# Optimization experiments

Hardware: AMD Instinct MI355X
Metric: run time of the kernel (lower is better)

Reference implementation:

```python
import jax, jax.numpy as jnp
import numpy as np

N = 50000
E = 800000
IN_CH = 128
HID = 32
HEADS = 8
OUT_CH = 64
NEG_SLOPE = 0.2


def _gat_layer(x, W, att_src, att_dst, bias, src, dst, H, C, concat):
    """One GATConv layer (add aggregation, self-loops appended).
    x: [n, Fin], W: [Fin, H*C], att_*: [H, C], bias: [H*C] or [C].
    src/dst: [E] int edge endpoints (no self loops; they are appended here).
    """
    n = x.shape[0]
    xs = (x @ W).reshape(n, H, C)                 # projected features [n,H,C]
    a_src = (xs * att_src).sum(-1)                # [n,H]
    a_dst = (xs * att_dst).sum(-1)                # [n,H]
    loop = jnp.arange(n, dtype=src.dtype)
    s = jnp.concatenate([src, loop])              # [E+n]
    d = jnp.concatenate([dst, loop])
    alpha = a_src[s] + a_dst[d]                   # per-edge score [E+n,H]
    alpha = jax.nn.leaky_relu(alpha, NEG_SLOPE)
    # segment softmax over destination node (every node has a self loop,
    # so no empty segments)
    amax = jax.ops.segment_max(alpha, d, num_segments=n)
    ex = jnp.exp(alpha - amax[d])
    denom = jax.ops.segment_sum(ex, d, num_segments=n)
    alpha = ex / denom[d]                         # normalized attention [E+n,H]
    # weighted scatter-add aggregation
    out = jax.ops.segment_sum(alpha[:, :, None] * xs[s], d, num_segments=n)
    out = out.reshape(n, H * C) if concat else out.mean(axis=1)
    return out + bias


def setup_inputs() -> dict:
    key = jax.random.key(0)
    ks = jax.random.split(key, 12)
    def glorot(k, shape):
        fan = shape[0] + shape[-1]
        return jax.random.uniform(k, shape, jnp.float32,
                                  -jnp.sqrt(6.0 / fan), jnp.sqrt(6.0 / fan))
    x = jax.random.normal(ks[0], (N, IN_CH), jnp.float32)
    edge_index = jax.random.randint(ks[1], (2, E), 0, N, dtype=jnp.int64)
    W1 = glorot(ks[2], (IN_CH, HEADS * HID))
    att_src1 = glorot(ks[3], (HEADS, HID))
    att_dst1 = glorot(ks[4], (HEADS, HID))
    bias1 = jnp.zeros((HEADS * HID,), jnp.float32)
    W2 = glorot(ks[5], (HEADS * HID, 1 * OUT_CH))
    att_src2 = glorot(ks[6], (1, OUT_CH))
    att_dst2 = glorot(ks[7], (1, OUT_CH))
    bias2 = jnp.zeros((OUT_CH,), jnp.float32)
    return {"x": x, "edge_index": edge_index,
            "W1": W1, "att_src1": att_src1, "att_dst1": att_dst1, "bias1": bias1,
            "W2": W2, "att_src2": att_src2, "att_dst2": att_dst2, "bias2": bias2}


def reference(x, edge_index, W1, att_src1, att_dst1, bias1,
              W2, att_src2, att_dst2, bias2):
    src, dst = edge_index[0], edge_index[1]
    h = _gat_layer(x, W1, att_src1, att_dst1, bias1, src, dst,
                   HEADS, HID, concat=True)      # [N, HEADS*HID]
    h = jax.nn.elu(h)
    out = _gat_layer(h, W2, att_src2, att_dst2, bias2, src, dst,
                     1, OUT_CH, concat=False)    # [N, OUT_CH]
    return out
```

## Files before the change

kernel.cpp:

```cpp
#include <hip/hip_runtime.h>

#define NN 50000
#define NE 800000
#define IN_CH 128
#define HID 32
#define HEADS 8
#define HC 256
#define OUT_CH 64
#define NEG_SLOPE 0.2f
#define SCAN_BLOCKS 196

typedef _Float16 half4 __attribute__((ext_vector_type(4)));
typedef _Float16 half8 __attribute__((ext_vector_type(8)));
typedef float    f32x4 __attribute__((ext_vector_type(4)));


__global__ void hist_kernel(const int* __restrict__ dst, int* __restrict__ deg) {
    int e = blockIdx.x * blockDim.x + threadIdx.x;
    if (e < NE) atomicAdd(&deg[dst[e]], 1);
}

__global__ __launch_bounds__(256)
void scan_phase1(const int* __restrict__ deg, int* __restrict__ excl,
                 int* __restrict__ bsum) {
    __shared__ int sm[256];
    const int t = blockIdx.x * 256 + threadIdx.x;
    const int v = (t < NN) ? deg[t] : 0;
    sm[threadIdx.x] = v;
    __syncthreads();
    for (int off = 1; off < 256; off <<= 1) {
        int u = (threadIdx.x >= off) ? sm[threadIdx.x - off] : 0;
        __syncthreads();
        sm[threadIdx.x] += u;
        __syncthreads();
    }
    if (t < NN) excl[t] = sm[threadIdx.x] - v;
    if (threadIdx.x == 255) bsum[blockIdx.x] = sm[255];
}

__global__ __launch_bounds__(256)
void scan_phase2(const int* __restrict__ bsum, int* __restrict__ boff,
                 int* __restrict__ offsets) {
    __shared__ int sm[256];
    const int t = threadIdx.x;
    const int v = (t < SCAN_BLOCKS) ? bsum[t] : 0;
    sm[t] = v;
    __syncthreads();
    for (int off = 1; off < 256; off <<= 1) {
        int u = (t >= off) ? sm[t - off] : 0;
        __syncthreads();
        sm[t] += u;
        __syncthreads();
    }
    if (t < SCAN_BLOCKS) boff[t] = sm[t] - v;
    if (t == 255) offsets[NN] = sm[255];
}

__global__ __launch_bounds__(256)
void scan_phase3(const int* __restrict__ excl, const int* __restrict__ boff,
                 int* __restrict__ offsets, int* __restrict__ cursor) {
    const int t = blockIdx.x * 256 + threadIdx.x;
    if (t < NN) {
        int v = excl[t] + boff[blockIdx.x];
        offsets[t] = v;
        cursor[t]  = v;
    }
}

__global__ void scatter_kernel(const int* __restrict__ src,
                               const int* __restrict__ dst,
                               int* __restrict__ cursor, int* __restrict__ ssrc) {
    int e = blockIdx.x * blockDim.x + threadIdx.x;
    if (e < NE) {
        int d = dst[e];
        int pos = atomicAdd(&cursor[d], 1);
        ssrc[pos] = src[e];
    }
}


__global__ void cast_f32_f16(const float* __restrict__ in, _Float16* __restrict__ out,
                             int n8) {
    int i = blockIdx.x * blockDim.x + threadIdx.x;
    if (i >= n8) return;
    float4 a = ((const float4*)in)[i * 2];
    float4 b = ((const float4*)in)[i * 2 + 1];
    half8 h;
    h[0] = (_Float16)a.x; h[1] = (_Float16)a.y; h[2] = (_Float16)a.z; h[3] = (_Float16)a.w;
    h[4] = (_Float16)b.x; h[5] = (_Float16)b.y; h[6] = (_Float16)b.z; h[7] = (_Float16)b.w;
    ((half8*)out)[i] = h;
}

__global__ void transpose_cast(const float* __restrict__ W, _Float16* __restrict__ Wt,
                               int K, int N) {
    int i = blockIdx.x * blockDim.x + threadIdx.x;
    if (i >= K * N) return;
    int k = i / N, n = i - k * N;
    Wt[(size_t)n * K + k] = (_Float16)W[i];
}

__global__ __launch_bounds__(256)
void gemm_mfma_h(const _Float16* __restrict__ A, const _Float16* __restrict__ Bt,
                 _Float16* __restrict__ C, int M, int N, int K) {
    __shared__ _Float16 Asl[64][136];
    __shared__ _Float16 Btl[64][136];
    const int tid  = threadIdx.x;
    const int wave = tid >> 6, lane = tid & 63;
    const int lr = lane & 15, lk = lane >> 4;
    const int bm = blockIdx.x * 64, bn = blockIdx.y * 64;
    const int sr = tid >> 2;
    const int ss = (tid & 3) * 32;

    f32x4 acc[4];
#pragma unroll
    for (int i = 0; i < 4; ++i) acc[i] = (f32x4){0.f, 0.f, 0.f, 0.f};

    for (int k0 = 0; k0 < K; k0 += 128) {
        {
            const int ar = bm + sr;
            half8 v0 = {}, v1 = {}, v2 = {}, v3 = {};
            if (ar < M) {
                const half8* ga = (const half8*)(A + (size_t)ar * K + k0 + ss);
                v0 = ga[0]; v1 = ga[1]; v2 = ga[2]; v3 = ga[3];
            }
            *(half8*)&Asl[sr][ss + 0]  = v0;
            *(half8*)&Asl[sr][ss + 8]  = v1;
            *(half8*)&Asl[sr][ss + 16] = v2;
            *(half8*)&Asl[sr][ss + 24] = v3;
            const half8* gb = (const half8*)(Bt + (size_t)(bn + sr) * K + k0 + ss);
            half8 w0 = gb[0], w1 = gb[1], w2 = gb[2], w3 = gb[3];
            *(half8*)&Btl[sr][ss + 0]  = w0;
            *(half8*)&Btl[sr][ss + 8]  = w1;
            *(half8*)&Btl[sr][ss + 16] = w2;
            *(half8*)&Btl[sr][ss + 24] = w3;
        }
        __syncthreads();
#pragma unroll
        for (int kk = 0; kk < 128; kk += 32) {
            half8 a = *(const half8*)&Asl[wave * 16 + lr][kk + lk * 8];
#pragma unroll
            for (int nt = 0; nt < 4; ++nt) {
                half8 b = *(const half8*)&Btl[nt * 16 + lr][kk + lk * 8];
                acc[nt] = __builtin_amdgcn_mfma_f32_16x16x32_f16(a, b, acc[nt], 0, 0, 0);
            }
        }
        __syncthreads();
    }
#pragma unroll
    for (int nt = 0; nt < 4; ++nt) {
        const int col = bn + nt * 16 + lr;
#pragma unroll
        for (int r = 0; r < 4; ++r) {
            const int m = bm + wave * 16 + lk * 4 + r;
            if (m < M) C[(size_t)m * N + col] = (_Float16)acc[nt][r];
        }
    }
}


__global__ void attcoef1(const _Float16* __restrict__ xs, const float* __restrict__ att_s,
                         const float* __restrict__ att_d,
                         float* __restrict__ a_s, float* __restrict__ a_d) {
    int idx = blockIdx.x * blockDim.x + threadIdx.x;
    if (idx >= NN * HEADS) return;
    int h = idx & 7;
    const _Float16* xp = xs + (long)idx * 32;
    const float* sp = att_s + h * 32;
    const float* dp = att_d + h * 32;
    float as = 0.f, ad = 0.f;
#pragma unroll
    for (int i = 0; i < 4; ++i) {
        half8 v = *(const half8*)(xp + i * 8);
#pragma unroll
        for (int j = 0; j < 8; ++j) {
            float f = (float)v[j];
            as += f * sp[i * 8 + j];
            ad += f * dp[i * 8 + j];
        }
    }
    a_s[idx] = as;
    a_d[idx] = ad;
}

__global__ void attcoef2(const _Float16* __restrict__ xs, const float* __restrict__ att_s,
                         const float* __restrict__ att_d,
                         float* __restrict__ a_s, float* __restrict__ a_d) {
    int n = blockIdx.x * blockDim.x + threadIdx.x;
    if (n >= NN) return;
    const _Float16* xp = xs + (long)n * 64;
    float as = 0.f, ad = 0.f;
#pragma unroll
    for (int i = 0; i < 8; ++i) {
        half8 v = *(const half8*)(xp + i * 8);
#pragma unroll
        for (int j = 0; j < 8; ++j) {
            float f = (float)v[j];
            as += f * att_s[i * 8 + j];
            ad += f * att_d[i * 8 + j];
        }
    }
    a_s[n] = as;
    a_d[n] = ad;
}


__device__ __forceinline__ float lrelu(float x) { return x > 0.f ? x : NEG_SLOPE * x; }

__global__ __launch_bounds__(256)
void agg1(const _Float16* __restrict__ xs, const float* __restrict__ a_s,
          const float* __restrict__ a_d, const int* __restrict__ offsets,
          const int* __restrict__ ssrc, const float* __restrict__ bias,
          _Float16* __restrict__ out) {
    __shared__ float pl_all[4][64 * 9];
    const int wslot = threadIdx.x >> 6;
    const int wave = (blockIdx.x * blockDim.x + threadIdx.x) >> 6;
    const int lane = threadIdx.x & 63;
    if (wave >= NN) return;
    float* pl = pl_all[wslot];
    const int n = wave;
    const int h = lane >> 3;
    const int ch = h * 32 + (lane & 7) * 4;

    const float4 D0 = *(const float4*)(a_d + (long)n * 8);
    const float4 D1 = *(const float4*)(a_d + (long)n * 8 + 4);
    const float adn = a_d[n * 8 + h];
    const int beg = offsets[n], end = offsets[n + 1];

    float pself = __expf(lrelu(a_s[n * 8 + h] + adn));
    float den = pself;
    float ax, ay, az, aw;
    {
        half4 v = *(const half4*)(xs + (long)n * HC + ch);
        ax = pself * (float)v[0]; ay = pself * (float)v[1];
        az = pself * (float)v[2]; aw = pself * (float)v[3];
    }

    for (int base = beg; base < end; base += 64) {
        const int cnt = min(64, end - base);
        int sidx = 0;
        if (lane < cnt) {
            sidx = ssrc[base + lane];
            const float4* ap = (const float4*)(a_s + (long)sidx * 8);
            float4 A0 = ap[0], A1 = ap[1];
            pl[lane * 9 + 0] = __expf(lrelu(A0.x + D0.x));
            pl[lane * 9 + 1] = __expf(lrelu(A0.y + D0.y));
            pl[lane * 9 + 2] = __expf(lrelu(A0.z + D0.z));
            pl[lane * 9 + 3] = __expf(lrelu(A0.w + D0.w));
            pl[lane * 9 + 4] = __expf(lrelu(A1.x + D1.x));
            pl[lane * 9 + 5] = __expf(lrelu(A1.y + D1.y));
            pl[lane * 9 + 6] = __expf(lrelu(A1.z + D1.z));
            pl[lane * 9 + 7] = __expf(lrelu(A1.w + D1.w));
        }
        asm volatile("s_waitcnt lgkmcnt(0)" ::: "memory");

        int u = 0;
        for (; u + 8 <= cnt; u += 8) {
            int s0 = __shfl(sidx, u + 0), s1 = __shfl(sidx, u + 1);
            int s2 = __shfl(sidx, u + 2), s3 = __shfl(sidx, u + 3);
            int s4 = __shfl(sidx, u + 4), s5 = __shfl(sidx, u + 5);
            int s6 = __shfl(sidx, u + 6), s7 = __shfl(sidx, u + 7);
            half4 v0 = *(const half4*)(xs + (long)s0 * HC + ch);
            half4 v1 = *(const half4*)(xs + (long)s1 * HC + ch);
            half4 v2 = *(const half4*)(xs + (long)s2 * HC + ch);
            half4 v3 = *(const half4*)(xs + (long)s3 * HC + ch);
            half4 v4 = *(const half4*)(xs + (long)s4 * HC + ch);
            half4 v5 = *(const half4*)(xs + (long)s5 * HC + ch);
            half4 v6 = *(const half4*)(xs + (long)s6 * HC + ch);
            half4 v7 = *(const half4*)(xs + (long)s7 * HC + ch);
            float p0 = pl[(u + 0) * 9 + h], p1 = pl[(u + 1) * 9 + h];
            float p2 = pl[(u + 2) * 9 + h], p3 = pl[(u + 3) * 9 + h];
            float p4 = pl[(u + 4) * 9 + h], p5 = pl[(u + 5) * 9 + h];
            float p6 = pl[(u + 6) * 9 + h], p7 = pl[(u + 7) * 9 + h];
            den += ((p0 + p1) + (p2 + p3)) + ((p4 + p5) + (p6 + p7));
            ax += p0 * (float)v0[0] + p1 * (float)v1[0] + p2 * (float)v2[0] + p3 * (float)v3[0]
                + p4 * (float)v4[0] + p5 * (float)v5[0] + p6 * (float)v6[0] + p7 * (float)v7[0];
            ay += p0 * (float)v0[1] + p1 * (float)v1[1] + p2 * (float)v2[1] + p3 * (float)v3[1]
                + p4 * (float)v4[1] + p5 * (float)v5[1] + p6 * (float)v6[1] + p7 * (float)v7[1];
            az += p0 * (float)v0[2] + p1 * (float)v1[2] + p2 * (float)v2[2] + p3 * (float)v3[2]
                + p4 * (float)v4[2] + p5 * (float)v5[2] + p6 * (float)v6[2] + p7 * (float)v7[2];
            aw += p0 * (float)v0[3] + p1 * (float)v1[3] + p2 * (float)v2[3] + p3 * (float)v3[3]
                + p4 * (float)v4[3] + p5 * (float)v5[3] + p6 * (float)v6[3] + p7 * (float)v7[3];
        }
        for (; u < cnt; ++u) {
            int s = __shfl(sidx, u);
            float p = pl[u * 9 + h];
            half4 v = *(const half4*)(xs + (long)s * HC + ch);
            den += p;
            ax += p * (float)v[0]; ay += p * (float)v[1];
            az += p * (float)v[2]; aw += p * (float)v[3];
        }
    }
    float inv = 1.0f / den;
    float4 b = *(const float4*)(bias + ch);
    float ox = ax * inv + b.x, oy = ay * inv + b.y;
    float oz = az * inv + b.z, ow = aw * inv + b.w;
    ox = ox > 0.f ? ox : expm1f(ox);
    oy = oy > 0.f ? oy : expm1f(oy);
    oz = oz > 0.f ? oz : expm1f(oz);
    ow = ow > 0.f ? ow : expm1f(ow);
    half4 ho;
    ho[0] = (_Float16)ox; ho[1] = (_Float16)oy;
    ho[2] = (_Float16)oz; ho[3] = (_Float16)ow;
    *(half4*)(out + (long)n * HC + ch) = ho;
}

__global__ __launch_bounds__(256)
void agg2(const _Float16* __restrict__ xs, const float* __restrict__ a_s,
          const float* __restrict__ a_d, const int* __restrict__ offsets,
          const int* __restrict__ ssrc, const float* __restrict__ bias,
          float* __restrict__ out) {
    const int wave = (blockIdx.x * blockDim.x + threadIdx.x) >> 6;
    const int lane = threadIdx.x & 63;
    if (wave >= NN) return;
    const int n = wave;

    const float adn = a_d[n];
    const int beg = offsets[n], end = offsets[n + 1];

    float pself = __expf(lrelu(a_s[n] + adn));
    float den = pself;
    float acc = pself * (float)xs[(long)n * OUT_CH + lane];

    for (int base = beg; base < end; base += 64) {
        const int cnt = min(64, end - base);
        int sidx = 0;
        float pe = 0.f;
        if (lane < cnt) {
            sidx = ssrc[base + lane];
            pe = __expf(lrelu(a_s[sidx] + adn));
        }
        int u = 0;
        for (; u + 8 <= cnt; u += 8) {
            int s0 = __shfl(sidx, u + 0), s1 = __shfl(sidx, u + 1);
            int s2 = __shfl(sidx, u + 2), s3 = __shfl(sidx, u + 3);
            int s4 = __shfl(sidx, u + 4), s5 = __shfl(sidx, u + 5);
            int s6 = __shfl(sidx, u + 6), s7 = __shfl(sidx, u + 7);
            float p0 = __shfl(pe, u + 0), p1 = __shfl(pe, u + 1);
            float p2 = __shfl(pe, u + 2), p3 = __shfl(pe, u + 3);
            float p4 = __shfl(pe, u + 4), p5 = __shfl(pe, u + 5);
            float p6 = __shfl(pe, u + 6), p7 = __shfl(pe, u + 7);
            float v0 = (float)xs[(long)s0 * OUT_CH + lane];
            float v1 = (float)xs[(long)s1 * OUT_CH + lane];
            float v2 = (float)xs[(long)s2 * OUT_CH + lane];
            float v3 = (float)xs[(long)s3 * OUT_CH + lane];
            float v4 = (float)xs[(long)s4 * OUT_CH + lane];
            float v5 = (float)xs[(long)s5 * OUT_CH + lane];
            float v6 = (float)xs[(long)s6 * OUT_CH + lane];
            float v7 = (float)xs[(long)s7 * OUT_CH + lane];
            den += ((p0 + p1) + (p2 + p3)) + ((p4 + p5) + (p6 + p7));
            acc += p0 * v0 + p1 * v1 + p2 * v2 + p3 * v3
                 + p4 * v4 + p5 * v5 + p6 * v6 + p7 * v7;
        }
        for (; u < cnt; ++u) {
            int s = __shfl(sidx, u);
            float p = __shfl(pe, u);
            den += p;
            acc += p * (float)xs[(long)s * OUT_CH + lane];
        }
    }
    out[(long)n * OUT_CH + lane] = acc / den + bias[lane];
}


extern "C" void kernel_launch(void* const* d_in, const int* in_sizes, int n_in,
                              void* d_out, int out_size, void* d_ws, size_t ws_size,
                              hipStream_t stream) {
    const float* x     = (const float*)d_in[0];
    const int*   ei    = (const int*)d_in[1];
    const float* W1    = (const float*)d_in[2];
    const float* atts1 = (const float*)d_in[3];
    const float* attd1 = (const float*)d_in[4];
    const float* bias1 = (const float*)d_in[5];
    const float* W2    = (const float*)d_in[6];
    const float* atts2 = (const float*)d_in[7];
    const float* attd2 = (const float*)d_in[8];
    const float* bias2 = (const float*)d_in[9];
    float*       out   = (float*)d_out;

    const int* srcp = ei;
    const int* dstp = ei + NE;

    char* ws = (char*)d_ws;
    size_t off = 0;
    auto alloc = [&](size_t bytes) -> void* {
        void* p = ws + off;
        off += (bytes + 255) & ~(size_t)255;
        return p;
    };
    _Float16* xh    = (_Float16*)alloc((size_t)NN * IN_CH * 2);
    _Float16* xs1h  = (_Float16*)alloc((size_t)NN * HC * 2);
    _Float16* h1h   = (_Float16*)alloc((size_t)NN * HC * 2);
    _Float16* W1t   = (_Float16*)alloc((size_t)HC * IN_CH * 2);
    _Float16* W2t   = (_Float16*)alloc((size_t)OUT_CH * HC * 2);
    float*    as1   = (float*)alloc((size_t)NN * HEADS * 4);
    float*    ad1   = (float*)alloc((size_t)NN * HEADS * 4);
    int*   deg      = (int*)alloc((size_t)NN * 4);
    int*   offsets  = (int*)alloc((size_t)(NN + 1) * 4);
    int*   cursor   = (int*)alloc((size_t)NN * 4);
    int*   ssrc     = (int*)alloc((size_t)NE * 4);
    int*   excl     = (int*)alloc((size_t)NN * 4);
    int*   bsum     = (int*)alloc((size_t)SCAN_BLOCKS * 4);
    int*   boff     = (int*)alloc((size_t)SCAN_BLOCKS * 4);
    _Float16* xs2h = xs1h;
    float*    as2  = as1;
    float*    ad2  = ad1;

    hipMemsetAsync(deg, 0, (size_t)NN * 4, stream);
    hist_kernel<<<(NE + 255) / 256, 256, 0, stream>>>(dstp, deg);
    scan_phase1<<<SCAN_BLOCKS, 256, 0, stream>>>(deg, excl, bsum);
    scan_phase2<<<1, 256, 0, stream>>>(bsum, boff, offsets);
    scan_phase3<<<SCAN_BLOCKS, 256, 0, stream>>>(excl, boff, offsets, cursor);
    scatter_kernel<<<(NE + 255) / 256, 256, 0, stream>>>(srcp, dstp, cursor, ssrc);

    cast_f32_f16<<<(NN * IN_CH / 8 + 255) / 256, 256, 0, stream>>>(x, xh, NN * IN_CH / 8);
    transpose_cast<<<(IN_CH * HC + 255) / 256, 256, 0, stream>>>(W1, W1t, IN_CH, HC);
    transpose_cast<<<(HC * OUT_CH + 255) / 256, 256, 0, stream>>>(W2, W2t, HC, OUT_CH);

    {
        dim3 grid((NN + 63) / 64, HC / 64);
        gemm_mfma_h<<<grid, 256, 0, stream>>>(xh, W1t, xs1h, NN, HC, IN_CH);
    }
    attcoef1<<<(NN * HEADS + 255) / 256, 256, 0, stream>>>(xs1h, atts1, attd1, as1, ad1);
    agg1<<<(NN + 3) / 4, 256, 0, stream>>>(xs1h, as1, ad1, offsets, ssrc, bias1, h1h);

    {
        dim3 grid((NN + 63) / 64, OUT_CH / 64);
        gemm_mfma_h<<<grid, 256, 0, stream>>>(h1h, W2t, xs2h, NN, OUT_CH, HC);
    }
    attcoef2<<<(NN + 255) / 256, 256, 0, stream>>>(xs2h, atts2, attd2, as2, ad2);
    agg2<<<(NN + 3) / 4, 256, 0, stream>>>(xs2h, as2, ad2, offsets, ssrc, bias2, out);
}
```

Measured before the change: 324.9 us.

## Store layer-1 features head-major and aggregate one head per wave

The layer-1 GEMM now writes its projected features head-major ([head][node][32]), and the attention coefficients are stored the same way. The aggregation kernel processes one head per wave instead of all eight, with 8 edges in flight per iteration split across lane groups and a cross-lane reduction at the end. Each head's gathers then touch a compact 3.2MB slice that fits better in cache. The cost is 8x more waves, repeated reads of offsets and source indices per head, and a shuffle reduction.

```diff
diff --git a/kernel.cpp b/kernel.cpp
--- a/kernel.cpp
+++ b/kernel.cpp
@@ -157,14 +157,73 @@
     }
 }
 
-
-__global__ void attcoef1(const _Float16* __restrict__ xs, const float* __restrict__ att_s,
+__global__ __launch_bounds__(256)
+void gemm_mfma_hm(const _Float16* __restrict__ A, const _Float16* __restrict__ Bt,
+                  _Float16* __restrict__ C, int M, int N, int K) {
+    __shared__ _Float16 Asl[64][136];
+    __shared__ _Float16 Btl[64][136];
+    const int tid  = threadIdx.x;
+    const int wave = tid >> 6, lane = tid & 63;
+    const int lr = lane & 15, lk = lane >> 4;
+    const int bm = blockIdx.x * 64, bn = blockIdx.y * 64;
+    const int sr = tid >> 2;
+    const int ss = (tid & 3) * 32;
+
+    f32x4 acc[4];
+#pragma unroll
+    for (int i = 0; i < 4; ++i) acc[i] = (f32x4){0.f, 0.f, 0.f, 0.f};
+
+    for (int k0 = 0; k0 < K; k0 += 128) {
+        {
+            const int ar = bm + sr;
+            half8 v0 = {}, v1 = {}, v2 = {}, v3 = {};
+            if (ar < M) {
+                const half8* ga = (const half8*)(A + (size_t)ar * K + k0 + ss);
+                v0 = ga[0]; v1 = ga[1]; v2 = ga[2]; v3 = ga[3];
+            }
+            *(half8*)&Asl[sr][ss + 0]  = v0;
+            *(half8*)&Asl[sr][ss + 8]  = v1;
+            *(half8*)&Asl[sr][ss + 16] = v2;
+            *(half8*)&Asl[sr][ss + 24] = v3;
+            const half8* gb = (const half8*)(Bt + (size_t)(bn + sr) * K + k0 + ss);
+            half8 w0 = gb[0], w1 = gb[1], w2 = gb[2], w3 = gb[3];
+            *(half8*)&Btl[sr][ss + 0]  = w0;
+            *(half8*)&Btl[sr][ss + 8]  = w1;
+            *(half8*)&Btl[sr][ss + 16] = w2;
+            *(half8*)&Btl[sr][ss + 24] = w3;
+        }
+        __syncthreads();
+#pragma unroll
+        for (int kk = 0; kk < 128; kk += 32) {
+            half8 a = *(const half8*)&Asl[wave * 16 + lr][kk + lk * 8];
+#pragma unroll
+            for (int nt = 0; nt < 4; ++nt) {
+                half8 b = *(const half8*)&Btl[nt * 16 + lr][kk + lk * 8];
+                acc[nt] = __builtin_amdgcn_mfma_f32_16x16x32_f16(a, b, acc[nt], 0, 0, 0);
+            }
+        }
+        __syncthreads();
+    }
+#pragma unroll
+    for (int nt = 0; nt < 4; ++nt) {
+        const int col = bn + nt * 16 + lr;
+        const int hh = col >> 5, cc = col & 31;
+#pragma unroll
+        for (int r = 0; r < 4; ++r) {
+            const int m = bm + wave * 16 + lk * 4 + r;
+            if (m < M) C[((size_t)hh * M + m) * 32 + cc] = (_Float16)acc[nt][r];
+        }
+    }
+}
+
+
+__global__ void attcoef1(const _Float16* __restrict__ xsh, const float* __restrict__ att_s,
                          const float* __restrict__ att_d,
-                         float* __restrict__ a_s, float* __restrict__ a_d) {
-    int idx = blockIdx.x * blockDim.x + threadIdx.x;
-    if (idx >= NN * HEADS) return;
-    int h = idx & 7;
-    const _Float16* xp = xs + (long)idx * 32;
+                         float* __restrict__ a_sh, float* __restrict__ a_dh) {
+    int n = blockIdx.x * blockDim.x + threadIdx.x;
+    int h = blockIdx.y;
+    if (n >= NN) return;
+    const _Float16* xp = xsh + ((size_t)h * NN + n) * 32;
     const float* sp = att_s + h * 32;
     const float* dp = att_d + h * 32;
     float as = 0.f, ad = 0.f;
@@ -178,8 +237,8 @@
             ad += f * dp[i * 8 + j];
         }
     }
-    a_s[idx] = as;
-    a_d[idx] = ad;
+    a_sh[(size_t)h * NN + n] = as;
+    a_dh[(size_t)h * NN + n] = ad;
 }
 
 __global__ void attcoef2(const _Float16* __restrict__ xs, const float* __restrict__ att_s,
@@ -207,101 +266,73 @@
 __device__ __forceinline__ float lrelu(float x) { return x > 0.f ? x : NEG_SLOPE * x; }
 
 __global__ __launch_bounds__(256)
-void agg1(const _Float16* __restrict__ xs, const float* __restrict__ a_s,
-          const float* __restrict__ a_d, const int* __restrict__ offsets,
-          const int* __restrict__ ssrc, const float* __restrict__ bias,
+void agg1(const _Float16* __restrict__ xsh,
+          const float* __restrict__ a_sh,
+          const float* __restrict__ a_dh,
+          const int* __restrict__ offsets, const int* __restrict__ ssrc,
+          const float* __restrict__ bias,
           _Float16* __restrict__ out) {
-    __shared__ float pl_all[4][64 * 9];
-    const int wslot = threadIdx.x >> 6;
-    const int wave = (blockIdx.x * blockDim.x + threadIdx.x) >> 6;
+    const int b = blockIdx.x;
+    const int head = b & 7;
+    const int wave = threadIdx.x >> 6;
     const int lane = threadIdx.x & 63;
-    if (wave >= NN) return;
-    float* pl = pl_all[wslot];
-    const int n = wave;
-    const int h = lane >> 3;
-    const int ch = h * 32 + (lane & 7) * 4;
-
-    const float4 D0 = *(const float4*)(a_d + (long)n * 8);
-    const float4 D1 = *(const float4*)(a_d + (long)n * 8 + 4);
-    const float adn = a_d[n * 8 + h];
+    const int n = (b >> 3) * 4 + wave;
+    if (n >= NN) return;
+    const int eslot = lane >> 3;
+    const int ch = (lane & 7) * 4;
+    const _Float16* xh = xsh + (size_t)head * NN * 32;
+    const float* ash = a_sh + (size_t)head * NN;
+
+    const float adn = a_dh[(size_t)head * NN + n];
     const int beg = offsets[n], end = offsets[n + 1];
 
-    float pself = __expf(lrelu(a_s[n * 8 + h] + adn));
-    float den = pself;
-    float ax, ay, az, aw;
-    {
-        half4 v = *(const half4*)(xs + (long)n * HC + ch);
-        ax = pself * (float)v[0]; ay = pself * (float)v[1];
-        az = pself * (float)v[2]; aw = pself * (float)v[3];
-    }
+    float den = 0.f, ax = 0.f, ay = 0.f, az = 0.f, aw = 0.f;
 
     for (int base = beg; base < end; base += 64) {
         const int cnt = min(64, end - base);
         int sidx = 0;
+        float pe = 0.f;
         if (lane < cnt) {
             sidx = ssrc[base + lane];
-            const float4* ap = (const float4*)(a_s + (long)sidx * 8);
-            float4 A0 = ap[0], A1 = ap[1];
-            pl[lane * 9 + 0] = __expf(lrelu(A0.x + D0.x));
-            pl[lane * 9 + 1] = __expf(lrelu(A0.y + D0.y));
-            pl[lane * 9 + 2] = __expf(lrelu(A0.z + D0.z));
-            pl[lane * 9 + 3] = __expf(lrelu(A0.w + D0.w));
-            pl[lane * 9 + 4] = __expf(lrelu(A1.x + D1.x));
-            pl[lane * 9 + 5] = __expf(lrelu(A1.y + D1.y));
-            pl[lane * 9 + 6] = __expf(lrelu(A1.z + D1.z));
-            pl[lane * 9 + 7] = __expf(lrelu(A1.w + D1.w));
-        }
-        asm volatile("s_waitcnt lgkmcnt(0)" ::: "memory");
-
-        int u = 0;
-        for (; u + 8 <= cnt; u += 8) {
-            int s0 = __shfl(sidx, u + 0), s1 = __shfl(sidx, u + 1);
-            int s2 = __shfl(sidx, u + 2), s3 = __shfl(sidx, u + 3);
-            int s4 = __shfl(sidx, u + 4), s5 = __shfl(sidx, u + 5);
-            int s6 = __shfl(sidx, u + 6), s7 = __shfl(sidx, u + 7);
-            half4 v0 = *(const half4*)(xs + (long)s0 * HC + ch);
-            half4 v1 = *(const half4*)(xs + (long)s1 * HC + ch);
-            half4 v2 = *(const half4*)(xs + (long)s2 * HC + ch);
-            half4 v3 = *(const half4*)(xs + (long)s3 * HC + ch);
-            half4 v4 = *(const half4*)(xs + (long)s4 * HC + ch);
-            half4 v5 = *(const half4*)(xs + (long)s5 * HC + ch);
-            half4 v6 = *(const half4*)(xs + (long)s6 * HC + ch);
-            half4 v7 = *(const half4*)(xs + (long)s7 * HC + ch);
-            float p0 = pl[(u + 0) * 9 + h], p1 = pl[(u + 1) * 9 + h];
-            float p2 = pl[(u + 2) * 9 + h], p3 = pl[(u + 3) * 9 + h];
-            float p4 = pl[(u + 4) * 9 + h], p5 = pl[(u + 5) * 9 + h];
-            float p6 = pl[(u + 6) * 9 + h], p7 = pl[(u + 7) * 9 + h];
-            den += ((p0 + p1) + (p2 + p3)) + ((p4 + p5) + (p6 + p7));
-            ax += p0 * (float)v0[0] + p1 * (float)v1[0] + p2 * (float)v2[0] + p3 * (float)v3[0]
-                + p4 * (float)v4[0] + p5 * (float)v5[0] + p6 * (float)v6[0] + p7 * (float)v7[0];
-            ay += p0 * (float)v0[1] + p1 * (float)v1[1] + p2 * (float)v2[1] + p3 * (float)v3[1]
-                + p4 * (float)v4[1] + p5 * (float)v5[1] + p6 * (float)v6[1] + p7 * (float)v7[1];
-            az += p0 * (float)v0[2] + p1 * (float)v1[2] + p2 * (float)v2[2] + p3 * (float)v3[2]
-                + p4 * (float)v4[2] + p5 * (float)v5[2] + p6 * (float)v6[2] + p7 * (float)v7[2];
-            aw += p0 * (float)v0[3] + p1 * (float)v1[3] + p2 * (float)v2[3] + p3 * (float)v3[3]
-                + p4 * (float)v4[3] + p5 * (float)v5[3] + p6 * (float)v6[3] + p7 * (float)v7[3];
-        }
-        for (; u < cnt; ++u) {
-            int s = __shfl(sidx, u);
-            float p = pl[u * 9 + h];
-            half4 v = *(const half4*)(xs + (long)s * HC + ch);
+            pe = __expf(lrelu(ash[sidx] + adn));
+        }
+        for (int u = 0; u * 8 < cnt; ++u) {
+            int   es = __shfl(sidx, u * 8 + eslot);
+            float p  = __shfl(pe,   u * 8 + eslot);
+            half4 v  = *(const half4*)(xh + (size_t)es * 32 + ch);
             den += p;
             ax += p * (float)v[0]; ay += p * (float)v[1];
             az += p * (float)v[2]; aw += p * (float)v[3];
         }
     }
-    float inv = 1.0f / den;
-    float4 b = *(const float4*)(bias + ch);
-    float ox = ax * inv + b.x, oy = ay * inv + b.y;
-    float oz = az * inv + b.z, ow = aw * inv + b.w;
-    ox = ox > 0.f ? ox : expm1f(ox);
-    oy = oy > 0.f ? oy : expm1f(oy);
-    oz = oz > 0.f ? oz : expm1f(oz);
-    ow = ow > 0.f ? ow : expm1f(ow);
-    half4 ho;
-    ho[0] = (_Float16)ox; ho[1] = (_Float16)oy;
-    ho[2] = (_Float16)oz; ho[3] = (_Float16)ow;
-    *(half4*)(out + (long)n * HC + ch) = ho;
+#pragma unroll
+    for (int m = 8; m <= 32; m <<= 1) {
+        den += __shfl_xor(den, m);
+        ax  += __shfl_xor(ax, m);
+        ay  += __shfl_xor(ay, m);
+        az  += __shfl_xor(az, m);
+        aw  += __shfl_xor(aw, m);
+    }
+    const float pself = __expf(lrelu(ash[n] + adn));
+    half4 sv = *(const half4*)(xh + (size_t)n * 32 + ch);
+    den += pself;
+    ax += pself * (float)sv[0]; ay += pself * (float)sv[1];
+    az += pself * (float)sv[2]; aw += pself * (float)sv[3];
+
+    if (eslot == 0) {
+        const float inv = 1.0f / den;
+        float4 bb = *(const float4*)(bias + head * 32 + ch);
+        float ox = ax * inv + bb.x, oy = ay * inv + bb.y;
+        float oz = az * inv + bb.z, ow = aw * inv + bb.w;
+        ox = ox > 0.f ? ox : expm1f(ox);
+        oy = oy > 0.f ? oy : expm1f(oy);
+        oz = oz > 0.f ? oz : expm1f(oz);
+        ow = ow > 0.f ? ow : expm1f(ow);
+        half4 ho;
+        ho[0] = (_Float16)ox; ho[1] = (_Float16)oy;
+        ho[2] = (_Float16)oz; ho[3] = (_Float16)ow;
+        *(half4*)(out + (size_t)n * HC + head * 32 + ch) = ho;
+    }
 }
 
 __global__ __launch_bounds__(256)
@@ -388,7 +419,7 @@
         return p;
     };
     _Float16* xh    = (_Float16*)alloc((size_t)NN * IN_CH * 2);
-    _Float16* xs1h  = (_Float16*)alloc((size_t)NN * HC * 2);
+    _Float16* xsh1  = (_Float16*)alloc((size_t)NN * HC * 2);
     _Float16* h1h   = (_Float16*)alloc((size_t)NN * HC * 2);
     _Float16* W1t   = (_Float16*)alloc((size_t)HC * IN_CH * 2);
     _Float16* W2t   = (_Float16*)alloc((size_t)OUT_CH * HC * 2);
@@ -401,7 +432,7 @@
     int*   excl     = (int*)alloc((size_t)NN * 4);
     int*   bsum     = (int*)alloc((size_t)SCAN_BLOCKS * 4);
     int*   boff     = (int*)alloc((size_t)SCAN_BLOCKS * 4);
-    _Float16* xs2h = xs1h;
+    _Float16* xs2h = xsh1;
     float*    as2  = as1;
     float*    ad2  = ad1;
 
@@ -418,10 +449,13 @@
 
     {
         dim3 grid((NN + 63) / 64, HC / 64);
-        gemm_mfma_h<<<grid, 256, 0, stream>>>(xh, W1t, xs1h, NN, HC, IN_CH);
-    }
-    attcoef1<<<(NN * HEADS + 255) / 256, 256, 0, stream>>>(xs1h, atts1, attd1, as1, ad1);
-    agg1<<<(NN + 3) / 4, 256, 0, stream>>>(xs1h, as1, ad1, offsets, ssrc, bias1, h1h);
+        gemm_mfma_hm<<<grid, 256, 0, stream>>>(xh, W1t, xsh1, NN, HC, IN_CH);
+    }
+    {
+        dim3 grid((NN + 255) / 256, HEADS);
+        attcoef1<<<grid, 256, 0, stream>>>(xsh1, atts1, attd1, as1, ad1);
+    }
+    agg1<<<((NN + 3) / 4) * 8, 256, 0, stream>>>(xsh1, as1, ad1, offsets, ssrc, bias1, h1h);
 
     {
         dim3 grid((NN + 63) / 64, OUT_CH / 64);
```

After: 414.3 us. 1.28x slower.
